# Kernel tuning notes

Hardware: AMD Instinct MI355X
Metric: run time of the kernel (lower is better)

## Reference

```python
import jax, jax.numpy as jnp
import numpy as np

B, T, D, P = 8, 2048, 768, 1024


def setup_inputs() -> dict:
    key = jax.random.key(0)
    kx, kp = jax.random.split(key)
    x = jax.random.normal(kx, (B, T, D), dtype=jnp.float32)
    prototypes = jax.random.normal(kp, (P, D), dtype=jnp.float32)
    return {"x": x, "prototypes": prototypes}


def reference(x, prototypes):
    # sum((x[...,None,:] - p)**2, -1) without the [B,T,P,D] intermediate)
    x_sq = jnp.sum(x * x, axis=-1, keepdims=True)          # [B,T,1]
    p_sq = jnp.sum(prototypes * prototypes, axis=-1)        # [P]
    cross = jnp.einsum("btd,pd->btp", x, prototypes)       # [B,T,P]
    distances = x_sq + p_sq[None, None, :] - 2.0 * cross    # [B,T,P]
    return distances, prototypes
```

## Files before the change

kernel.cpp:

```cpp
#include <hip/hip_runtime.h>
#include <hip/hip_bf16.h>
#include <stdint.h>

#define M_ROWS 16384
#define N_COLS 1024
#define K_DIM  768
#define NKT    12

typedef __attribute__((ext_vector_type(8))) short bf16x8;
typedef __attribute__((ext_vector_type(4))) float f32x4;

__device__ __forceinline__ void async_copy16(void* lds, const void* g) {
  __builtin_amdgcn_global_load_lds(
      (const __attribute__((address_space(1))) unsigned int*)g,
      (__attribute__((address_space(3))) unsigned int*)lds,
      16, 0, 0);
}

__device__ __forceinline__ unsigned short f2bf(float f) {
  __hip_bfloat16 h = __float2bfloat16(f);
  return *reinterpret_cast<unsigned short*>(&h);
}

__global__ void prep_all(const float* __restrict__ x,
                         const float* __restrict__ p,
                         unsigned short* __restrict__ xb,
                         unsigned short* __restrict__ pbu,
                         float* __restrict__ xsq,
                         float* __restrict__ psq,
                         float* __restrict__ proto_out) {
  const int b = blockIdx.x;
  const int wid = threadIdx.x >> 6;
  const int lane = threadIdx.x & 63;
  const float* src;
  unsigned short* dst;
  float* sq;
  float* cp;
  int row;
  if (b < M_ROWS / 4) {
    row = b * 4 + wid;
    src = x; dst = xb; sq = xsq; cp = nullptr;
  } else {
    row = (b - M_ROWS / 4) * 4 + wid;
    src = p; dst = pbu; sq = psq; cp = proto_out;
  }
  const float4* r = (const float4*)(src + (size_t)row * K_DIM);
  ushort4* rb = (ushort4*)(dst + (size_t)row * K_DIM);
  float4* cpv = cp ? (float4*)(cp + (size_t)row * K_DIM) : nullptr;
  float acc = 0.f;
#pragma unroll
  for (int i = 0; i < 3; ++i) {
    float4 v = r[i * 64 + lane];
    acc += v.x * v.x + v.y * v.y + v.z * v.z + v.w * v.w;
    ushort4 u;
    u.x = f2bf(v.x); u.y = f2bf(v.y); u.z = f2bf(v.z); u.w = f2bf(v.w);
    rb[i * 64 + lane] = u;
    if (cpv) cpv[i * 64 + lane] = v;
  }
#pragma unroll
  for (int off = 32; off; off >>= 1) acc += __shfl_down(acc, off);
  if (lane == 0) sq[row] = acc;
}

__device__ __forceinline__ bf16x8 ldsfrag(const char* tile, int row, int slot) {
  return *(const bf16x8*)(tile + row * 128 + (((slot ^ (row & 7)) << 4)));
}

__global__ __launch_bounds__(256, 2) void dist_gemm(
    const __hip_bfloat16* __restrict__ xb,
    const __hip_bfloat16* __restrict__ pb,
    const float* __restrict__ xsq,
    const float* __restrict__ psq,
    float* __restrict__ out) {
  __shared__ char lds[2][2][16384];

  const int flat = blockIdx.x;
  const int xcd = flat & 7;
  const int local = flat >> 3;
  const int bm = xcd * 16 + (local >> 3);
  const int bn = local & 7;

  const int tid = threadIdx.x;
  const int wave = tid >> 6;
  const int lane = tid & 63;
  const int wm = wave >> 1;
  const int wn = wave & 1;
  const int rl = lane & 15;
  const int kq = lane >> 4;

  f32x4 acc[4][4] = {};
  bf16x8 af[4][2], bfr[4][2];

  const __hip_bfloat16* Abase = xb + (size_t)(bm * 128) * K_DIM;
  const __hip_bfloat16* Bbase = pb + (size_t)(bn * 128) * K_DIM;

  int gofs[4];
#pragma unroll
  for (int c = 0; c < 4; ++c) {
    const int row = c * 32 + (tid >> 3);
    const int g = (tid & 7) ^ (row & 7);
    gofs[c] = row * K_DIM + g * 8;
  }

#define STAGE(buf, ktile)                                                   \
  do {                                                                      \
    _Pragma("unroll") for (int c = 0; c < 4; ++c) {                         \
      const int lofs = (c * 256 + tid) * 16;                                \
      async_copy16(&lds[buf][0][0] + lofs, Abase + gofs[c] + (ktile) * 64); \
      async_copy16(&lds[buf][1][0] + lofs, Bbase + gofs[c] + (ktile) * 64); \
    }                                                                       \
  } while (0)

  STAGE(0, 0);
  asm volatile("s_waitcnt vmcnt(0)" ::: "memory");
  asm volatile("s_barrier" ::: "memory");

  for (int kt = 0; kt < NKT; ++kt) {
    const int cur = kt & 1;
    if (kt + 1 < NKT) STAGE(cur ^ 1, kt + 1);

    const char* At = &lds[cur][0][0];
    const char* Bt = &lds[cur][1][0];
#pragma unroll
    for (int mi = 0; mi < 4; ++mi)
#pragma unroll
      for (int kk = 0; kk < 2; ++kk)
        af[mi][kk] = ldsfrag(At, wm * 64 + mi * 16 + rl, kk * 4 + kq);
#pragma unroll
    for (int ni = 0; ni < 4; ++ni)
#pragma unroll
      for (int kk = 0; kk < 2; ++kk)
        bfr[ni][kk] = ldsfrag(Bt, wn * 64 + ni * 16 + rl, kk * 4 + kq);

    __builtin_amdgcn_s_setprio(1);
#pragma unroll
    for (int mi = 0; mi < 4; ++mi)
#pragma unroll
      for (int ni = 0; ni < 4; ++ni)
#pragma unroll
        for (int kk = 0; kk < 2; ++kk)
          acc[mi][ni] = __builtin_amdgcn_mfma_f32_16x16x32_bf16(
              af[mi][kk], bfr[ni][kk], acc[mi][ni], 0, 0, 0);
    __builtin_amdgcn_s_setprio(0);

    asm volatile("s_waitcnt vmcnt(0)" ::: "memory");
    asm volatile("s_barrier" ::: "memory");
  }
#undef STAGE

  const int c0 = bn * 128 + wn * 64;
  const int r0 = bm * 128 + wm * 64;
#pragma unroll
  for (int mi = 0; mi < 4; ++mi) {
#pragma unroll
    for (int ni = 0; ni < 4; ++ni) {
      const int col = c0 + ni * 16 + rl;
      const float ps = psq[col];
#pragma unroll
      for (int r = 0; r < 4; ++r) {
        const int row = r0 + mi * 16 + kq * 4 + r;
        out[(size_t)row * N_COLS + col] = xsq[row] + ps - 2.0f * acc[mi][ni][r];
      }
    }
  }
}

extern "C" void kernel_launch(void* const* d_in, const int* in_sizes, int n_in,
                              void* d_out, int out_size, void* d_ws, size_t ws_size,
                              hipStream_t stream) {
  const float* x = (const float*)d_in[0];
  const float* p = (const float*)d_in[1];
  float* out = (float*)d_out;
  char* ws = (char*)d_ws;

  float* xsq = (float*)ws;
  float* psq = (float*)(ws + 65536);
  unsigned short* xb = (unsigned short*)(ws + 69632);
  unsigned short* pbu = xb + (size_t)M_ROWS * K_DIM;
  float* proto_out = out + (size_t)M_ROWS * N_COLS;

  prep_all<<<M_ROWS / 4 + N_COLS / 4, 256, 0, stream>>>(x, p, xb, pbu, xsq,
                                                        psq, proto_out);

  dist_gemm<<<1024, 256, 0, stream>>>((const __hip_bfloat16*)xb,
                                      (const __hip_bfloat16*)pbu,
                                      xsq, psq, out);
}
```

Baseline: 47.16 us.

## Fuse x bf16 conversion and row-norm computation into the distance GEMM

The prep kernel no longer converts x to bf16 or computes ||x||^2. The GEMM now streams fp32 x tiles into LDS, converts them to bf16 in registers, and accumulates the row sums of squares on the fly, reducing them into shared memory before the epilogue. K-tiles shrink to 32 so the fp32 A tile fits, which doubles the number of k iterations and barriers. This removes a full write and re-read of the bf16 x copy, but each x tile is loaded in fp32 by all 8 column blocks, doubling A traffic from L2, and adds conversion ALU work in the inner loop.

```diff
diff --git a/kernel.cpp b/kernel.cpp
--- a/kernel.cpp
+++ b/kernel.cpp
@@ -5,7 +5,7 @@
 #define M_ROWS 16384
 #define N_COLS 1024
 #define K_DIM  768
-#define NKT    12
+#define NKT    24
 
 typedef __attribute__((ext_vector_type(8))) short bf16x8;
 typedef __attribute__((ext_vector_type(4))) float f32x4;
@@ -17,36 +17,26 @@
       16, 0, 0);
 }
 
+__device__ __forceinline__ short b16(float f) {
+  __hip_bfloat16 h = __float2bfloat16(f);
+  return *reinterpret_cast<short*>(&h);
+}
+
 __device__ __forceinline__ unsigned short f2bf(float f) {
   __hip_bfloat16 h = __float2bfloat16(f);
   return *reinterpret_cast<unsigned short*>(&h);
 }
 
-__global__ void prep_all(const float* __restrict__ x,
-                         const float* __restrict__ p,
-                         unsigned short* __restrict__ xb,
-                         unsigned short* __restrict__ pbu,
-                         float* __restrict__ xsq,
-                         float* __restrict__ psq,
-                         float* __restrict__ proto_out) {
-  const int b = blockIdx.x;
+__global__ void prep_rows(const float* __restrict__ src,
+                          unsigned short* __restrict__ dstb,
+                          float* __restrict__ sq,
+                          float* __restrict__ copy_out) {
   const int wid = threadIdx.x >> 6;
   const int lane = threadIdx.x & 63;
-  const float* src;
-  unsigned short* dst;
-  float* sq;
-  float* cp;
-  int row;
-  if (b < M_ROWS / 4) {
-    row = b * 4 + wid;
-    src = x; dst = xb; sq = xsq; cp = nullptr;
-  } else {
-    row = (b - M_ROWS / 4) * 4 + wid;
-    src = p; dst = pbu; sq = psq; cp = proto_out;
-  }
+  const int row = blockIdx.x * 4 + wid;
   const float4* r = (const float4*)(src + (size_t)row * K_DIM);
-  ushort4* rb = (ushort4*)(dst + (size_t)row * K_DIM);
-  float4* cpv = cp ? (float4*)(cp + (size_t)row * K_DIM) : nullptr;
+  ushort4* rb = (ushort4*)(dstb + (size_t)row * K_DIM);
+  float4* cp = (float4*)(copy_out + (size_t)row * K_DIM);
   float acc = 0.f;
 #pragma unroll
   for (int i = 0; i < 3; ++i) {
@@ -55,24 +45,21 @@
     ushort4 u;
     u.x = f2bf(v.x); u.y = f2bf(v.y); u.z = f2bf(v.z); u.w = f2bf(v.w);
     rb[i * 64 + lane] = u;
-    if (cpv) cpv[i * 64 + lane] = v;
+    cp[i * 64 + lane] = v;
   }
 #pragma unroll
   for (int off = 32; off; off >>= 1) acc += __shfl_down(acc, off);
   if (lane == 0) sq[row] = acc;
 }
 
-__device__ __forceinline__ bf16x8 ldsfrag(const char* tile, int row, int slot) {
-  return *(const bf16x8*)(tile + row * 128 + (((slot ^ (row & 7)) << 4)));
-}
-
 __global__ __launch_bounds__(256, 2) void dist_gemm(
-    const __hip_bfloat16* __restrict__ xb,
+    const float* __restrict__ x,
     const __hip_bfloat16* __restrict__ pb,
-    const float* __restrict__ xsq,
     const float* __restrict__ psq,
     float* __restrict__ out) {
-  __shared__ char lds[2][2][16384];
+  __shared__ char ldsA[2][16384];
+  __shared__ char ldsB[2][8192];
+  __shared__ float xsq_s[128];
 
   const int flat = blockIdx.x;
   const int xcd = flat & 7;
@@ -89,26 +76,34 @@
   const int kq = lane >> 4;
 
   f32x4 acc[4][4] = {};
-  bf16x8 af[4][2], bfr[4][2];
-
-  const __hip_bfloat16* Abase = xb + (size_t)(bm * 128) * K_DIM;
+  float ssq[4] = {0.f, 0.f, 0.f, 0.f};
+
+  const float* Abase = x + (size_t)(bm * 128) * K_DIM;
   const __hip_bfloat16* Bbase = pb + (size_t)(bn * 128) * K_DIM;
 
-  int gofs[4];
+  int agofs[4];
 #pragma unroll
   for (int c = 0; c < 4; ++c) {
     const int row = c * 32 + (tid >> 3);
     const int g = (tid & 7) ^ (row & 7);
-    gofs[c] = row * K_DIM + g * 8;
-  }
-
-#define STAGE(buf, ktile)                                                   \
-  do {                                                                      \
-    _Pragma("unroll") for (int c = 0; c < 4; ++c) {                         \
-      const int lofs = (c * 256 + tid) * 16;                                \
-      async_copy16(&lds[buf][0][0] + lofs, Abase + gofs[c] + (ktile) * 64); \
-      async_copy16(&lds[buf][1][0] + lofs, Bbase + gofs[c] + (ktile) * 64); \
-    }                                                                       \
+    agofs[c] = row * K_DIM + g * 4;
+  }
+  int bgofs[2];
+#pragma unroll
+  for (int c = 0; c < 2; ++c) {
+    const int row = c * 64 + (tid >> 2);
+    const int g = (tid & 3) ^ ((row >> 1) & 3);
+    bgofs[c] = row * K_DIM + g * 8;
+  }
+
+#define STAGE(buf, ktile)                                                    \
+  do {                                                                       \
+    _Pragma("unroll") for (int c = 0; c < 4; ++c)                            \
+        async_copy16(&ldsA[buf][(c * 256 + tid) * 16],                       \
+                     Abase + agofs[c] + (ktile) * 32);                       \
+    _Pragma("unroll") for (int c = 0; c < 2; ++c)                            \
+        async_copy16(&ldsB[buf][(c * 256 + tid) * 16],                       \
+                     Bbase + bgofs[c] + (ktile) * 32);                       \
   } while (0)
 
   STAGE(0, 0);
@@ -119,28 +114,39 @@
     const int cur = kt & 1;
     if (kt + 1 < NKT) STAGE(cur ^ 1, kt + 1);
 
-    const char* At = &lds[cur][0][0];
-    const char* Bt = &lds[cur][1][0];
+    const char* At = &ldsA[cur][0];
+    const char* Bt = &ldsB[cur][0];
+
+    bf16x8 af[4], bfr[4];
+#pragma unroll
+    for (int mi = 0; mi < 4; ++mi) {
+      const int r = wm * 64 + mi * 16 + rl;
+      const int s0 = (2 * kq) ^ (r & 7);
+      f32x4 lo = *(const f32x4*)(At + r * 128 + s0 * 16);
+      f32x4 hi = *(const f32x4*)(At + r * 128 + (s0 ^ 1) * 16);
+      bf16x8 v;
+      v[0] = b16(lo[0]); v[1] = b16(lo[1]); v[2] = b16(lo[2]); v[3] = b16(lo[3]);
+      v[4] = b16(hi[0]); v[5] = b16(hi[1]); v[6] = b16(hi[2]); v[7] = b16(hi[3]);
+      af[mi] = v;
+      if (wn == 0)
+        ssq[mi] += lo[0] * lo[0] + lo[1] * lo[1] + lo[2] * lo[2] +
+                   lo[3] * lo[3] + hi[0] * hi[0] + hi[1] * hi[1] +
+                   hi[2] * hi[2] + hi[3] * hi[3];
+    }
+#pragma unroll
+    for (int ni = 0; ni < 4; ++ni) {
+      const int r = wn * 64 + ni * 16 + rl;
+      const int s = kq ^ ((r >> 1) & 3);
+      bfr[ni] = *(const bf16x8*)(Bt + r * 64 + s * 16);
+    }
+
+    __builtin_amdgcn_s_setprio(1);
 #pragma unroll
     for (int mi = 0; mi < 4; ++mi)
 #pragma unroll
-      for (int kk = 0; kk < 2; ++kk)
-        af[mi][kk] = ldsfrag(At, wm * 64 + mi * 16 + rl, kk * 4 + kq);
-#pragma unroll
-    for (int ni = 0; ni < 4; ++ni)
-#pragma unroll
-      for (int kk = 0; kk < 2; ++kk)
-        bfr[ni][kk] = ldsfrag(Bt, wn * 64 + ni * 16 + rl, kk * 4 + kq);
-
-    __builtin_amdgcn_s_setprio(1);
-#pragma unroll
-    for (int mi = 0; mi < 4; ++mi)
-#pragma unroll
       for (int ni = 0; ni < 4; ++ni)
-#pragma unroll
-        for (int kk = 0; kk < 2; ++kk)
-          acc[mi][ni] = __builtin_amdgcn_mfma_f32_16x16x32_bf16(
-              af[mi][kk], bfr[ni][kk], acc[mi][ni], 0, 0, 0);
+        acc[mi][ni] = __builtin_amdgcn_mfma_f32_16x16x32_bf16(
+            af[mi], bfr[ni], acc[mi][ni], 0, 0, 0);
     __builtin_amdgcn_s_setprio(0);
 
     asm volatile("s_waitcnt vmcnt(0)" ::: "memory");
@@ -148,8 +154,20 @@
   }
 #undef STAGE
 
+  if (wn == 0) {
+#pragma unroll
+    for (int mi = 0; mi < 4; ++mi) {
+      ssq[mi] += __shfl_xor(ssq[mi], 16);
+      ssq[mi] += __shfl_xor(ssq[mi], 32);
+    }
+    if (lane < 16) {
+#pragma unroll
+      for (int mi = 0; mi < 4; ++mi) xsq_s[wm * 64 + mi * 16 + lane] = ssq[mi];
+    }
+  }
+  __syncthreads();
+
   const int c0 = bn * 128 + wn * 64;
-  const int r0 = bm * 128 + wm * 64;
 #pragma unroll
   for (int mi = 0; mi < 4; ++mi) {
 #pragma unroll
@@ -158,8 +176,9 @@
       const float ps = psq[col];
 #pragma unroll
       for (int r = 0; r < 4; ++r) {
-        const int row = r0 + mi * 16 + kq * 4 + r;
-        out[(size_t)row * N_COLS + col] = xsq[row] + ps - 2.0f * acc[mi][ni][r];
+        const int rloc = wm * 64 + mi * 16 + kq * 4 + r;
+        out[(size_t)(bm * 128 + rloc) * N_COLS + col] =
+            xsq_s[rloc] + ps - 2.0f * acc[mi][ni][r];
       }
     }
   }
@@ -173,16 +192,12 @@
   float* out = (float*)d_out;
   char* ws = (char*)d_ws;
 
-  float* xsq = (float*)ws;
-  float* psq = (float*)(ws + 65536);
-  unsigned short* xb = (unsigned short*)(ws + 69632);
-  unsigned short* pbu = xb + (size_t)M_ROWS * K_DIM;
+  float* psq = (float*)ws;
+  unsigned short* pbu = (unsigned short*)(ws + 4096);
   float* proto_out = out + (size_t)M_ROWS * N_COLS;
 
-  prep_all<<<M_ROWS / 4 + N_COLS / 4, 256, 0, stream>>>(x, p, xb, pbu, xsq,
-                                                        psq, proto_out);
-
-  dist_gemm<<<1024, 256, 0, stream>>>((const __hip_bfloat16*)xb,
-                                      (const __hip_bfloat16*)pbu,
-                                      xsq, psq, out);
-}
+  prep_rows<<<N_COLS / 4, 256, 0, stream>>>(p, pbu, psq, proto_out);
+
+  dist_gemm<<<1024, 256, 0, stream>>>(x, (const __hip_bfloat16*)pbu,
+                                      psq, out);
+}
```

New measurement: 67.23 us. +42.6%, slower.
